# Kernel optimization log

Hardware: AMD Instinct MI355X
Metric: run time of the kernel (lower is better)

## Reference

```python
import jax, jax.numpy as jnp
import numpy as np

N, E, C_IN, C_OUT, K = 50000, 800000, 64, 64, 3

def setup_inputs() -> dict:
    key = jax.random.key(0)
    k1, k2, k3, k4, k5, k6 = jax.random.split(key, 6)
    x = jax.random.normal(k1, (N, C_IN), dtype=jnp.float32)
    row = jax.random.randint(k2, (E,), 0, N)
    col = jax.random.randint(k3, (E,), 0, N)
    # PyG ChebConv removes self loops; avoid generating them
    col = jnp.where(col == row, (col + 1) % N, col)
    edge_index = jnp.stack([row, col])
    edge_weight = jax.random.uniform(k4, (E,), dtype=jnp.float32)
    # ChebConv learned params: one [C_in, C_out] matrix per Chebyshev order, plus bias
    W = jax.random.normal(k5, (K, C_IN, C_OUT), dtype=jnp.float32) / np.sqrt(C_IN).astype(np.float32)
    b = jax.random.normal(k6, (C_OUT,), dtype=jnp.float32) * 0.01
    return {"x": x, "edge_index": edge_index, "edge_weight": edge_weight, "W": W, "b": b}


def reference(x, edge_index, edge_weight, W, b):
    row, col = edge_index[0], edge_index[1]
    # PyG ChebConv.__norm__ with sym normalization and lambda_max = 2.0:
    # L_hat = (2/lambda_max) * (I - D^{-1/2} A D^{-1/2}) - I = -D^{-1/2} A D^{-1/2}
    deg = jax.ops.segment_sum(edge_weight, row, num_segments=N)
    dis = jnp.where(deg > 0, jax.lax.rsqrt(deg), 0.0)  # deg_inv_sqrt, inf -> 0
    w = -dis[row] * edge_weight * dis[col]             # [E] normalized Laplacian weights

    def prop(h):  # sparse matvec: L_hat @ h, [N, C]
        return jax.ops.segment_sum(w[:, None] * h[col], row, num_segments=N)

    # Chebyshev recurrence: T0 = x, T1 = L_hat x, Tk = 2 L_hat T_{k-1} - T_{k-2}
    Tx0 = x
    out = Tx0 @ W[0]
    Tx1 = prop(Tx0)
    out = out + Tx1 @ W[1]
    for k in range(2, K):
        Tx2 = 2.0 * prop(Tx1) - Tx0
        out = out + Tx2 @ W[k]
        Tx0, Tx1 = Tx1, Tx2
    return jax.nn.relu(out + b)
```

## Files before the change

### kernel.cpp

```cpp
#include <hip/hip_runtime.h>
#include <hip/hip_bf16.h>

#define C 64
#define NCOPY 8
#define FXSCALE 16777216.0f
#define LOW44 ((1ULL << 44) - 1)

typedef unsigned short u16;

__device__ __forceinline__ u16 f2bf_rne(float v) {
    unsigned u = __float_as_uint(v);
    u += 0x7FFFu + ((u >> 16) & 1u);
    return (u16)(u >> 16);
}
__device__ __forceinline__ float bf2f(u16 u) {
    return __uint_as_float((unsigned)u << 16);
}

__global__ __launch_bounds__(256) void hist8_kernel(const int* __restrict__ row,
                                                    const float* __restrict__ ew,
                                                    unsigned long long* __restrict__ cd8,
                                                    int* __restrict__ rank,
                                                    const float* __restrict__ x,
                                                    u16* __restrict__ xh,
                                                    int E, int N, int total4, int nthreads) {
    int t = threadIdx.x;
    int base = blockIdx.x * 1024;
    int copy = blockIdx.x & (NCOPY - 1);
    size_t cb = (size_t)copy * N;

    unsigned long long old[4];
    int e[4];
#pragma unroll
    for (int u = 0; u < 4; u++) {
        e[u] = base + u * 256 + t;
        if (e[u] < E) {
            int r = row[e[u]];
            unsigned long long fx = (unsigned long long)__float2uint_rn(ew[e[u]] * FXSCALE);
            unsigned long long inc = (1ULL << 44) | fx;
            old[u] = atomicAdd(&cd8[cb + r], inc);
        }
    }
#pragma unroll
    for (int u = 0; u < 4; u++) {
        if (e[u] < E) rank[e[u]] = (int)(old[u] >> 44);
    }

    int gtid = blockIdx.x * 256 + t;
    for (int i = gtid; i < total4; i += nthreads) {
        float4 v = *(const float4*)(x + (size_t)i * 4);
        ushort4 o;
        o.x = f2bf_rne(v.x); o.y = f2bf_rne(v.y);
        o.z = f2bf_rne(v.z); o.w = f2bf_rne(v.w);
        *(ushort4*)(xh + (size_t)i * 4) = o;
    }
}

__global__ __launch_bounds__(256) void scanA_kernel(const unsigned long long* __restrict__ cd8,
                                                    int* __restrict__ cnt,
                                                    float* __restrict__ dis,
                                                    int* __restrict__ bsum, int N) {
    __shared__ int s[256];
    int t = threadIdx.x;
    int i = blockIdx.x * 256 + t;
    int cv = 0;
    unsigned long long dfx = 0;
    if (i < N) {
#pragma unroll
        for (int c = 0; c < NCOPY; c++) {
            unsigned long long v = cd8[(size_t)c * N + i];
            cv += (int)(v >> 44);
            dfx += (v & LOW44);
        }
        cnt[i] = cv;
        float dv = (float)dfx * (1.0f / FXSCALE);
        dis[i] = (dv > 0.0f) ? rsqrtf(dv) : 0.0f;
    }
    s[t] = cv;
    __syncthreads();
    for (int off = 128; off > 0; off >>= 1) {
        if (t < off) s[t] += s[t + off];
        __syncthreads();
    }
    if (t == 0) bsum[blockIdx.x] = s[0];
}

__global__ __launch_bounds__(256) void scanB_kernel(int* __restrict__ bsum,
                                                    int* __restrict__ rowptr,
                                                    int G, int N) {
    __shared__ int s[256];
    int t = threadIdx.x;
    int v = (t < G) ? bsum[t] : 0;
    s[t] = v;
    __syncthreads();
    for (int off = 1; off < 256; off <<= 1) {
        int u = (t >= off) ? s[t - off] : 0;
        __syncthreads();
        s[t] += u;
        __syncthreads();
    }
    if (t < G) bsum[t] = s[t] - v;
    if (t == 255) rowptr[N] = s[255];
}

__global__ __launch_bounds__(256) void scanC_kernel(const int* __restrict__ cnt,
                                                    const unsigned long long* __restrict__ cd8,
                                                    int* __restrict__ start8,
                                                    const int* __restrict__ bsum,
                                                    int* __restrict__ rowptr, int N) {
    __shared__ int s[256];
    int t = threadIdx.x;
    int i = blockIdx.x * 256 + t;
    int v = (i < N) ? cnt[i] : 0;
    s[t] = v;
    __syncthreads();
    for (int off = 1; off < 256; off <<= 1) {
        int u = (t >= off) ? s[t - off] : 0;
        __syncthreads();
        s[t] += u;
        __syncthreads();
    }
    if (i < N) {
        int rp = bsum[blockIdx.x] + s[t] - v;
        rowptr[i] = rp;
        int run = rp;
#pragma unroll
        for (int c = 0; c < NCOPY; c++) {
            int tmp = (int)(cd8[(size_t)c * N + i] >> 44);
            start8[(size_t)c * N + i] = run;
            run += tmp;
        }
    }
}

__global__ __launch_bounds__(256) void scatter_kernel(const int* __restrict__ row,
                                                      const int* __restrict__ col,
                                                      const float* __restrict__ ew,
                                                      const float* __restrict__ dis,
                                                      const int* __restrict__ start8,
                                                      const int* __restrict__ rank,
                                                      float2* __restrict__ ewc,
                                                      int E, int N) {
    int t = threadIdx.x;
    int base = blockIdx.x * 1024;
    int copy = blockIdx.x & (NCOPY - 1);
    size_t cb = (size_t)copy * N;
#pragma unroll
    for (int u = 0; u < 4; u++) {
        int e = base + u * 256 + t;
        if (e < E) {
            int r = row[e];
            int c = col[e];
            float wv = -dis[r] * ew[e] * dis[c];
            int pos = start8[cb + r] + rank[e];
            ewc[pos] = make_float2(wv, __int_as_float(c));
        }
    }
}

__global__ __launch_bounds__(256) void spmm_csr_kernel(
        const int* __restrict__ rowptr,
        const float2* __restrict__ ewc,
        const unsigned* __restrict__ h32,
        float* __restrict__ out32,
        unsigned* __restrict__ outbf,
        int N) {
    int wid = (blockIdx.x * blockDim.x + threadIdx.x) >> 6;
    int lane = threadIdx.x & 63;
    if (wid >= N) return;
    int half = lane >> 5;
    int cp   = lane & 31;
    int beg = rowptr[wid];
    int end = rowptr[wid + 1];
    float ax0 = 0.f, ay0 = 0.f, ax1 = 0.f, ay1 = 0.f;
    float ax2 = 0.f, ay2 = 0.f, ax3 = 0.f, ay3 = 0.f;
    for (int base = beg; base < end; base += 64) {
        int idx = base + lane;
        float2 ed = (idx < end) ? ewc[idx] : make_float2(0.0f, __int_as_float(0));
        int cnt = end - base; if (cnt > 64) cnt = 64;
        for (int j = 0; j < cnt; j += 8) {
            int s0 = j + half;
            int s1 = j + 2 + half;
            int s2 = j + 4 + half;
            int s3 = j + 6 + half;
            float w0 = __shfl(ed.x, s0);
            int   c0 = __shfl(__float_as_int(ed.y), s0);
            float w1 = __shfl(ed.x, s1);
            int   c1 = __shfl(__float_as_int(ed.y), s1);
            float w2 = __shfl(ed.x, s2);
            int   c2 = __shfl(__float_as_int(ed.y), s2);
            float w3 = __shfl(ed.x, s3);
            int   c3 = __shfl(__float_as_int(ed.y), s3);
            unsigned hv0 = h32[(size_t)c0 * 32 + cp];
            unsigned hv1 = h32[(size_t)c1 * 32 + cp];
            unsigned hv2 = h32[(size_t)c2 * 32 + cp];
            unsigned hv3 = h32[(size_t)c3 * 32 + cp];
            ax0 = fmaf(w0, bf2f((u16)(hv0 & 0xffffu)), ax0);
            ay0 = fmaf(w0, bf2f((u16)(hv0 >> 16)),     ay0);
            ax1 = fmaf(w1, bf2f((u16)(hv1 & 0xffffu)), ax1);
            ay1 = fmaf(w1, bf2f((u16)(hv1 >> 16)),     ay1);
            ax2 = fmaf(w2, bf2f((u16)(hv2 & 0xffffu)), ax2);
            ay2 = fmaf(w2, bf2f((u16)(hv2 >> 16)),     ay2);
            ax3 = fmaf(w3, bf2f((u16)(hv3 & 0xffffu)), ax3);
            ay3 = fmaf(w3, bf2f((u16)(hv3 >> 16)),     ay3);
        }
    }
    float ax = (ax0 + ax1) + (ax2 + ax3);
    float ay = (ay0 + ay1) + (ay2 + ay3);
    float bx = __shfl(ax, cp + 32);
    float by = __shfl(ay, cp + 32);
    if (half == 0) {
        float rx = ax + bx;
        float ry = ay + by;
        *(float2*)(out32 + (size_t)wid * C + 2 * cp) = make_float2(rx, ry);
        unsigned pk = (unsigned)f2bf_rne(rx) | ((unsigned)f2bf_rne(ry) << 16);
        outbf[(size_t)wid * 32 + cp] = pk;
    }
}

__global__ __launch_bounds__(256) void final_gemm_kernel(
        const float* __restrict__ x,
        const float* __restrict__ T1,
        const float* __restrict__ P,
        const float* __restrict__ W,
        const float* __restrict__ b,
        float* __restrict__ out, int N) {
    __shared__ float As[16][64];
    __shared__ float Ws[16][64];

    int t  = threadIdx.x;
    int tx = t & 15;
    int ty = t >> 4;
    int n0 = blockIdx.x * 64;

    int sn = t >> 2;
    int skb = (t & 3) * 4;

    float acc[4][4];
#pragma unroll
    for (int i = 0; i < 4; i++)
#pragma unroll
        for (int j = 0; j < 4; j++) acc[i][j] = 0.0f;

#pragma unroll 1
    for (int s = 0; s < 12; s++) {
        float4 wv = *(const float4*)(W + s * 1024 + t * 4);
        int nn = n0 + sn;
        float4 av = make_float4(0.f, 0.f, 0.f, 0.f);
        if (nn < N) {
            if (s < 4) {
                av = *(const float4*)(x + (size_t)nn * C + s * 16 + skb);
            } else if (s < 8) {
                av = *(const float4*)(T1 + (size_t)nn * C + (s - 4) * 16 + skb);
            } else {
                float4 pv = *(const float4*)(P + (size_t)nn * C + (s - 8) * 16 + skb);
                float4 xv = *(const float4*)(x + (size_t)nn * C + (s - 8) * 16 + skb);
                av = make_float4(2.0f * pv.x - xv.x, 2.0f * pv.y - xv.y,
                                 2.0f * pv.z - xv.z, 2.0f * pv.w - xv.w);
            }
        }
        __syncthreads();
        {
            int wk = (t * 4) >> 6;
            int wc = (t * 4) & 63;
            *(float4*)&Ws[wk][wc] = wv;
        }
        As[skb + 0][sn] = av.x;
        As[skb + 1][sn] = av.y;
        As[skb + 2][sn] = av.z;
        As[skb + 3][sn] = av.w;
        __syncthreads();

#pragma unroll
        for (int kk = 0; kk < 16; kk++) {
            float4 a4 = *(const float4*)&As[kk][ty * 4];
            float4 w4 = *(const float4*)&Ws[kk][tx * 4];
            float ar[4] = {a4.x, a4.y, a4.z, a4.w};
            float wr[4] = {w4.x, w4.y, w4.z, w4.w};
#pragma unroll
            for (int i = 0; i < 4; i++)
#pragma unroll
                for (int j = 0; j < 4; j++)
                    acc[i][j] = fmaf(ar[i], wr[j], acc[i][j]);
        }
    }

    float4 bv = *(const float4*)(b + tx * 4);
    float br[4] = {bv.x, bv.y, bv.z, bv.w};
#pragma unroll
    for (int i = 0; i < 4; i++) {
        int node = n0 + ty * 4 + i;
        if (node < N) {
            float4 o;
            o.x = fmaxf(acc[i][0] + br[0], 0.0f);
            o.y = fmaxf(acc[i][1] + br[1], 0.0f);
            o.z = fmaxf(acc[i][2] + br[2], 0.0f);
            o.w = fmaxf(acc[i][3] + br[3], 0.0f);
            *(float4*)(out + (size_t)node * C + tx * 4) = o;
        }
    }
}

extern "C" void kernel_launch(void* const* d_in, const int* in_sizes, int n_in,
                              void* d_out, int out_size, void* d_ws, size_t ws_size,
                              hipStream_t stream) {
    const float* x  = (const float*)d_in[0];
    const int*   ei = (const int*)d_in[1];
    const float* ew = (const float*)d_in[2];
    const float* W  = (const float*)d_in[3];
    const float* b  = (const float*)d_in[4];
    float* out = (float*)d_out;

    const int N = in_sizes[0] / C;
    const int E = in_sizes[2];
    const int* row = ei;
    const int* col = ei + E;

    char* ws = (char*)d_ws;
    size_t off = 0;
    auto alloc = [&](size_t bytes) {
        void* p = ws + off;
        off = (off + bytes + 255) & ~(size_t)255;
        return p;
    };
    float*  dis    = (float*)alloc((size_t)N * 4);
    int*    cnt    = (int*)alloc((size_t)N * 4);
    int*    rowptr = (int*)alloc((size_t)(N + 1) * 4);
    float2* ewc    = (float2*)alloc((size_t)E * 8);
    float*  T1     = (float*)alloc((size_t)N * C * 4);
    float*  P      = (float*)alloc((size_t)N * C * 4);
    int*    bsum   = (int*)alloc((size_t)256 * 4);
    unsigned long long* cd8 = (unsigned long long*)alloc((size_t)NCOPY * N * 8);
    int*    start8 = (int*)alloc((size_t)NCOPY * N * 4);
    int*    rank   = (int*)alloc((size_t)E * 4);
    u16*    xh     = (u16*)alloc((size_t)N * C * 2);
    u16*    T1h    = (u16*)alloc((size_t)N * C * 2);
    u16*    Ph     = (u16*)alloc((size_t)N * C * 2);

    hipMemsetAsync(cd8, 0, (size_t)NCOPY * N * 8, stream);

    const int B = 256;
    const int G = (N + B - 1) / B;

    int histBlocks = (E + 1023) / 1024;
    int total4 = N * C / 4;
    hist8_kernel<<<histBlocks, B, 0, stream>>>(row, ew, cd8, rank, x, xh,
                                               E, N, total4, histBlocks * B);
    scanA_kernel<<<G, B, 0, stream>>>(cd8, cnt, dis, bsum, N);
    scanB_kernel<<<1, B, 0, stream>>>(bsum, rowptr, G, N);
    scanC_kernel<<<G, B, 0, stream>>>(cnt, cd8, start8, bsum, rowptr, N);
    scatter_kernel<<<histBlocks, B, 0, stream>>>(row, col, ew, dis, start8,
                                                 rank, ewc, E, N);

    int spmm_blocks = (int)(((long long)N * 64 + B - 1) / B);
    spmm_csr_kernel<<<spmm_blocks, B, 0, stream>>>(rowptr, ewc, (const unsigned*)xh,
                                                   T1, (unsigned*)T1h, N);
    spmm_csr_kernel<<<spmm_blocks, B, 0, stream>>>(rowptr, ewc, (const unsigned*)T1h,
                                                   P, (unsigned*)Ph, N);

    final_gemm_kernel<<<(N + 63) / 64, B, 0, stream>>>(x, T1, P, W, b, out, N);
}
```

Measured before the change: 205.5 us.

## Factor symmetric normalization out of edges and pack edge data into 32 bits

Moves the D^{-1/2} factors out of the per-edge weights. The source features are pre-scaled by dis when converted to bf16, and the destination is scaled by -dis in the SpMM epilogue. Each edge is stored as a 32-bit word (16-bit column index plus bf16 raw weight) instead of a float2, and rank is stored as u16. This halves the edge-stream traffic and removes the dis gathers in scatter. The 16-bit column packing only holds when N is at most 65536, and rank16 overflows beyond 65535 edges per row. The bf16 edge weights also reduce accuracy.

```diff
diff --git a/kernel.cpp b/kernel.cpp
--- a/kernel.cpp
+++ b/kernel.cpp
@@ -20,10 +20,8 @@
 __global__ __launch_bounds__(256) void hist8_kernel(const int* __restrict__ row,
                                                     const float* __restrict__ ew,
                                                     unsigned long long* __restrict__ cd8,
-                                                    int* __restrict__ rank,
-                                                    const float* __restrict__ x,
-                                                    u16* __restrict__ xh,
-                                                    int E, int N, int total4, int nthreads) {
+                                                    u16* __restrict__ rank16,
+                                                    int E, int N) {
     int t = threadIdx.x;
     int base = blockIdx.x * 1024;
     int copy = blockIdx.x & (NCOPY - 1);
@@ -43,16 +41,7 @@
     }
 #pragma unroll
     for (int u = 0; u < 4; u++) {
-        if (e[u] < E) rank[e[u]] = (int)(old[u] >> 44);
-    }
-
-    int gtid = blockIdx.x * 256 + t;
-    for (int i = gtid; i < total4; i += nthreads) {
-        float4 v = *(const float4*)(x + (size_t)i * 4);
-        ushort4 o;
-        o.x = f2bf_rne(v.x); o.y = f2bf_rne(v.y);
-        o.z = f2bf_rne(v.z); o.w = f2bf_rne(v.w);
-        *(ushort4*)(xh + (size_t)i * 4) = o;
+        if (e[u] < E) rank16[e[u]] = (u16)(old[u] >> 44);
     }
 }
 
@@ -107,11 +96,17 @@
                                                     const unsigned long long* __restrict__ cd8,
                                                     int* __restrict__ start8,
                                                     const int* __restrict__ bsum,
-                                                    int* __restrict__ rowptr, int N) {
+                                                    int* __restrict__ rowptr,
+                                                    const float* __restrict__ dis,
+                                                    const float* __restrict__ x,
+                                                    u16* __restrict__ xg,
+                                                    int N) {
     __shared__ int s[256];
+    __shared__ float sdis[256];
     int t = threadIdx.x;
     int i = blockIdx.x * 256 + t;
     int v = (i < N) ? cnt[i] : 0;
+    if (i < N) sdis[t] = dis[i];
     s[t] = v;
     __syncthreads();
     for (int off = 1; off < 256; off <<= 1) {
@@ -131,15 +126,29 @@
             run += tmp;
         }
     }
+    size_t nb = (size_t)blockIdx.x * 16384;
+#pragma unroll 1
+    for (int it = 0; it < 16; it++) {
+        int idx4 = it * 256 + t;
+        int lr = idx4 >> 4;
+        int gr = blockIdx.x * 256 + lr;
+        if (gr < N) {
+            float4 vv = *(const float4*)(x + nb + (size_t)idx4 * 4);
+            float di = sdis[lr];
+            ushort4 o;
+            o.x = f2bf_rne(vv.x * di); o.y = f2bf_rne(vv.y * di);
+            o.z = f2bf_rne(vv.z * di); o.w = f2bf_rne(vv.w * di);
+            *(ushort4*)(xg + nb + (size_t)idx4 * 4) = o;
+        }
+    }
 }
 
 __global__ __launch_bounds__(256) void scatter_kernel(const int* __restrict__ row,
                                                       const int* __restrict__ col,
                                                       const float* __restrict__ ew,
-                                                      const float* __restrict__ dis,
                                                       const int* __restrict__ start8,
-                                                      const int* __restrict__ rank,
-                                                      float2* __restrict__ ewc,
+                                                      const u16* __restrict__ rank16,
+                                                      unsigned* __restrict__ epk,
                                                       int E, int N) {
     int t = threadIdx.x;
     int base = blockIdx.x * 1024;
@@ -150,21 +159,21 @@
         int e = base + u * 256 + t;
         if (e < E) {
             int r = row[e];
-            int c = col[e];
-            float wv = -dis[r] * ew[e] * dis[c];
-            int pos = start8[cb + r] + rank[e];
-            ewc[pos] = make_float2(wv, __int_as_float(c));
+            unsigned pk = ((unsigned)col[e] << 16) | (unsigned)f2bf_rne(ew[e]);
+            int pos = start8[cb + r] + (int)rank16[e];
+            epk[pos] = pk;
         }
     }
 }
 
 __global__ __launch_bounds__(256) void spmm_csr_kernel(
         const int* __restrict__ rowptr,
-        const float2* __restrict__ ewc,
+        const unsigned* __restrict__ epk,
+        const float* __restrict__ dis,
         const unsigned* __restrict__ h32,
         float* __restrict__ out32,
         unsigned* __restrict__ outbf,
-        int N) {
+        int N, int writebf) {
     int wid = (blockIdx.x * blockDim.x + threadIdx.x) >> 6;
     int lane = threadIdx.x & 63;
     if (wid >= N) return;
@@ -176,21 +185,17 @@
     float ax2 = 0.f, ay2 = 0.f, ax3 = 0.f, ay3 = 0.f;
     for (int base = beg; base < end; base += 64) {
         int idx = base + lane;
-        float2 ed = (idx < end) ? ewc[idx] : make_float2(0.0f, __int_as_float(0));
+        unsigned ed = (idx < end) ? epk[idx] : 0u;
         int cnt = end - base; if (cnt > 64) cnt = 64;
         for (int j = 0; j < cnt; j += 8) {
-            int s0 = j + half;
-            int s1 = j + 2 + half;
-            int s2 = j + 4 + half;
-            int s3 = j + 6 + half;
-            float w0 = __shfl(ed.x, s0);
-            int   c0 = __shfl(__float_as_int(ed.y), s0);
-            float w1 = __shfl(ed.x, s1);
-            int   c1 = __shfl(__float_as_int(ed.y), s1);
-            float w2 = __shfl(ed.x, s2);
-            int   c2 = __shfl(__float_as_int(ed.y), s2);
-            float w3 = __shfl(ed.x, s3);
-            int   c3 = __shfl(__float_as_int(ed.y), s3);
+            unsigned e0 = (unsigned)__shfl((int)ed, j + half);
+            unsigned e1 = (unsigned)__shfl((int)ed, j + 2 + half);
+            unsigned e2 = (unsigned)__shfl((int)ed, j + 4 + half);
+            unsigned e3 = (unsigned)__shfl((int)ed, j + 6 + half);
+            float w0 = bf2f((u16)(e0 & 0xffffu)); int c0 = (int)(e0 >> 16);
+            float w1 = bf2f((u16)(e1 & 0xffffu)); int c1 = (int)(e1 >> 16);
+            float w2 = bf2f((u16)(e2 & 0xffffu)); int c2 = (int)(e2 >> 16);
+            float w3 = bf2f((u16)(e3 & 0xffffu)); int c3 = (int)(e3 >> 16);
             unsigned hv0 = h32[(size_t)c0 * 32 + cp];
             unsigned hv1 = h32[(size_t)c1 * 32 + cp];
             unsigned hv2 = h32[(size_t)c2 * 32 + cp];
@@ -210,11 +215,14 @@
     float bx = __shfl(ax, cp + 32);
     float by = __shfl(ay, cp + 32);
     if (half == 0) {
-        float rx = ax + bx;
-        float ry = ay + by;
+        float dr = dis[wid];
+        float rx = -dr * (ax + bx);
+        float ry = -dr * (ay + by);
         *(float2*)(out32 + (size_t)wid * C + 2 * cp) = make_float2(rx, ry);
-        unsigned pk = (unsigned)f2bf_rne(rx) | ((unsigned)f2bf_rne(ry) << 16);
-        outbf[(size_t)wid * 32 + cp] = pk;
+        if (writebf) {
+            unsigned pk = (unsigned)f2bf_rne(dr * rx) | ((unsigned)f2bf_rne(dr * ry) << 16);
+            outbf[(size_t)wid * 32 + cp] = pk;
+        }
     }
 }
 
@@ -323,19 +331,18 @@
         off = (off + bytes + 255) & ~(size_t)255;
         return p;
     };
-    float*  dis    = (float*)alloc((size_t)N * 4);
-    int*    cnt    = (int*)alloc((size_t)N * 4);
-    int*    rowptr = (int*)alloc((size_t)(N + 1) * 4);
-    float2* ewc    = (float2*)alloc((size_t)E * 8);
-    float*  T1     = (float*)alloc((size_t)N * C * 4);
-    float*  P      = (float*)alloc((size_t)N * C * 4);
-    int*    bsum   = (int*)alloc((size_t)256 * 4);
+    float*    dis    = (float*)alloc((size_t)N * 4);
+    int*      cnt    = (int*)alloc((size_t)N * 4);
+    int*      rowptr = (int*)alloc((size_t)(N + 1) * 4);
+    unsigned* epk    = (unsigned*)alloc((size_t)E * 4);
+    float*    T1     = (float*)alloc((size_t)N * C * 4);
+    float*    P      = (float*)alloc((size_t)N * C * 4);
+    int*      bsum   = (int*)alloc((size_t)256 * 4);
     unsigned long long* cd8 = (unsigned long long*)alloc((size_t)NCOPY * N * 8);
-    int*    start8 = (int*)alloc((size_t)NCOPY * N * 4);
-    int*    rank   = (int*)alloc((size_t)E * 4);
-    u16*    xh     = (u16*)alloc((size_t)N * C * 2);
-    u16*    T1h    = (u16*)alloc((size_t)N * C * 2);
-    u16*    Ph     = (u16*)alloc((size_t)N * C * 2);
+    int*      start8 = (int*)alloc((size_t)NCOPY * N * 4);
+    u16*      rank16 = (u16*)alloc((size_t)E * 2);
+    u16*      xg     = (u16*)alloc((size_t)N * C * 2);
+    u16*      T1g    = (u16*)alloc((size_t)N * C * 2);
 
     hipMemsetAsync(cd8, 0, (size_t)NCOPY * N * 8, stream);
 
@@ -343,20 +350,21 @@
     const int G = (N + B - 1) / B;
 
     int histBlocks = (E + 1023) / 1024;
-    int total4 = N * C / 4;
-    hist8_kernel<<<histBlocks, B, 0, stream>>>(row, ew, cd8, rank, x, xh,
-                                               E, N, total4, histBlocks * B);
+    hist8_kernel<<<histBlocks, B, 0, stream>>>(row, ew, cd8, rank16, E, N);
     scanA_kernel<<<G, B, 0, stream>>>(cd8, cnt, dis, bsum, N);
     scanB_kernel<<<1, B, 0, stream>>>(bsum, rowptr, G, N);
-    scanC_kernel<<<G, B, 0, stream>>>(cnt, cd8, start8, bsum, rowptr, N);
-    scatter_kernel<<<histBlocks, B, 0, stream>>>(row, col, ew, dis, start8,
-                                                 rank, ewc, E, N);
+    scanC_kernel<<<G, B, 0, stream>>>(cnt, cd8, start8, bsum, rowptr,
+                                      dis, x, xg, N);
+    scatter_kernel<<<histBlocks, B, 0, stream>>>(row, col, ew, start8,
+                                                 rank16, epk, E, N);
 
     int spmm_blocks = (int)(((long long)N * 64 + B - 1) / B);
-    spmm_csr_kernel<<<spmm_blocks, B, 0, stream>>>(rowptr, ewc, (const unsigned*)xh,
-                                                   T1, (unsigned*)T1h, N);
-    spmm_csr_kernel<<<spmm_blocks, B, 0, stream>>>(rowptr, ewc, (const unsigned*)T1h,
-                                                   P, (unsigned*)Ph, N);
+    spmm_csr_kernel<<<spmm_blocks, B, 0, stream>>>(rowptr, epk, dis,
+                                                   (const unsigned*)xg,
+                                                   T1, (unsigned*)T1g, N, 1);
+    spmm_csr_kernel<<<spmm_blocks, B, 0, stream>>>(rowptr, epk, dis,
+                                                   (const unsigned*)T1g,
+                                                   P, (unsigned*)T1g, N, 0);
 
     final_gemm_kernel<<<(N + 63) / 64, B, 0, stream>>>(x, T1, P, W, b, out, N);
 }
```

After: 205.7 us. No clear change (+0.1%).
